# Optimization experiments

Hardware: AMD Instinct MI355X
Metric: run time of the kernel (lower is better)

## Reference

```python
import jax, jax.numpy as jnp
import numpy as np

B = 2
NUM_CLS = 20
NUM_DIM = 256
H = W = 448
FH = FW = 28
K_TOP = 25


def _l2norm(x, eps=1e-12):
    # matches torch F.normalize(dim=1): x / max(||x||, eps); zero rows stay zero
    return x / jnp.maximum(jnp.linalg.norm(x, axis=-1, keepdims=True), eps)


def setup_inputs():
    key = jax.random.key(0)
    k1, k2, k3, k4 = jax.random.split(key, 4)
    fmap = jax.random.normal(k1, (B, NUM_DIM, FH, FW), jnp.float32)
    cam = jax.random.uniform(k2, (B, NUM_CLS, H, W), jnp.float32)
    cls_label = jax.random.randint(k3, (B, NUM_CLS), 0, 2).astype(jnp.float32)
    proj_weight = jax.random.normal(k4, (NUM_CLS, NUM_DIM), jnp.float32) * 0.02
    feature_contrast = jnp.zeros((NUM_CLS, NUM_DIM), jnp.float32)
    return {"fmap": fmap, "cam": cam, "cls_label": cls_label,
            "proj_weight": proj_weight, "feature_contrast": feature_contrast,
            "hig_thre": 0.7, "low_thre": 0.25, "bg_thre": 0.5}


def _forward(fmap, cam, cls_label, proj_weight, feature_contrast, hig_thre, low_thre, bg_thre):
    b, c, h, w = cam.shape
    d = fmap.shape[1]
    dt = fmap.dtype

    # ---- pseudo-label generation (vectorized over b,h,w) ----
    valid_cam = cls_label[:, :, None, None] * cam                       # [B,C,H,W]
    top2_v, top2_i = jax.lax.top_k(jnp.moveaxis(valid_cam, 1, -1), 2)   # [B,H,W,2]
    top1, second = top2_v[..., 0], top2_v[..., 1]
    pseudo = top2_i[..., 0] + 1
    pseudo = jnp.where(top1 < hig_thre, 255, pseudo)
    pseudo = jnp.where(top1 < low_thre, 0, pseudo)
    pseudo = jnp.where(top1 < bg_thre, 0, pseudo)
    pseudo = jnp.where((top1 - second < 0.3) & (top1 > hig_thre), 255, pseudo)

    # ---- upsample features (bilinear, align_corners=False) ----
    fmap_up = jax.image.resize(fmap, (b, d, h, w), 'bilinear')
    fmap_flat = fmap_up.reshape(b, d, h * w)                            # [B,D,HW]
    pseudo_flat = pseudo.reshape(b, h * w)                              # [B,HW]

    # ---- per-class features, both branches computed densely then selected ----
    cls_ids = jnp.arange(c) + 1
    mask = (pseudo_flat[:, None, :] == cls_ids[None, :, None]).astype(dt)  # [B,C,HW]
    counts = mask.sum(-1)                                                  # [B,C]
    feat_mask = jnp.einsum('bcp,bdp->bcd', mask, fmap_flat) / jnp.maximum(counts, 1.0)[:, :, None]
    _, top_idx = jax.lax.top_k(valid_cam.reshape(b, c, h * w), K_TOP)      # [B,C,25]
    gathered = jnp.take_along_axis(fmap_flat[:, None, :, :], top_idx[:, :, None, :], axis=-1)  # [B,C,D,25]
    feat_topk = gathered.mean(-1)                                          # [B,C,D]
    present = cls_label > 0.5                                              # [B,C] bool
    fsm = jnp.where((counts == 0.0)[:, :, None], feat_topk, feat_mask) * present[:, :, None]

    eye_f = jnp.eye(c, dtype=dt)
    eye_b = jnp.eye(c, dtype=bool)

    # ---- sequential per-sample loop (EMA memory bank carried across batch) ----
    def step(carry, xs):
        fc, loss_cls, loss_ccf = carry
        fsm_i, present_i = xs                                    # [C,D], [C]
        fsm_n = _l2norm(fsm_i)
        fc_n = _l2norm(jax.lax.stop_gradient(fc))
        cos = jnp.clip(jnp.abs(fsm_n @ fc_n.T), 1e-5, 1.0 - 1e-5)  # [C,C]
        ident = jnp.diag(present_i.astype(dt))
        loss_ccf = loss_ccf - (ident * jnp.log(cos) + (1.0 - ident) * jnp.log1p(-cos)).mean()
        off_max = jnp.where(eye_b, -jnp.inf, cos).max(axis=1)      # max over j != c
        qualify = present_i & (off_max < 0.6)                      # [C] bool
        p = jax.nn.softmax(fsm_i @ proj_weight.T, axis=-1)         # [C,C]
        logp = jnp.maximum(jnp.log(p), -100.0)
        log1mp = jnp.maximum(jnp.log1p(-p), -100.0)
        term = -(eye_f * logp + (1.0 - eye_f) * log1mp).mean(axis=-1)  # BCE(softmax, onehot) per class
        loss_cls = loss_cls + jnp.sum(jnp.where(qualify, term, 0.0))
        n = qualify.sum().astype(dt)
        loss_cls = jnp.where(n > 0, loss_cls / jnp.maximum(n, 1.0), loss_cls)
        fc = jnp.where(qualify[:, None], 0.95 * fc + 0.05 * jax.lax.stop_gradient(fsm_i), fc)
        return (fc, loss_cls, loss_ccf), None

    zero = jnp.asarray(0.0, dt)
    (_, loss_cls, loss_ccf), _ = jax.lax.scan(step, (feature_contrast, zero, zero), (fsm, present))
    return loss_ccf + loss_cls


def reference(fmap, cam, cls_label, proj_weight, feature_contrast, hig_thre, low_thre, bg_thre):
    return _forward(fmap, cam, cls_label, proj_weight, feature_contrast, hig_thre, low_thre, bg_thre)
```

## Files before the change

### kernel.cpp

```cpp
#include <hip/hip_runtime.h>
#include <cstdint>

#define HW 200704
#define IMG_W 448
#define NCLS 20
#define NDIM 256
#define NB2 784
#define LK 260

#define ASYNC_COPY16(gp, lp)                                                   \
  __builtin_amdgcn_global_load_lds(                                            \
      (const __attribute__((address_space(1))) void*)(gp),                     \
      (__attribute__((address_space(3))) void*)(lp), 16, 0, 0)

__global__ __launch_bounds__(256) void k_front(const float* __restrict__ fmap,
                                               float* __restrict__ fmapT,
                                               const float* __restrict__ cam,
                                               const float* __restrict__ cls_label,
                                               const float* __restrict__ hig_p,
                                               const float* __restrict__ low_p,
                                               const float* __restrict__ bg_p,
                                               float* __restrict__ W) {
  __shared__ float sT[NCLS][256];
  __shared__ int presList[NCLS];
  __shared__ int sNP;
  int tid = threadIdx.x;

  if (blockIdx.x >= 2 * NB2) {
    float (*tile)[33] = (float (*)[33]) & sT[0][0];
    int blk = blockIdx.x - 2 * NB2;
    int b = blk / 200;
    int t = blk % 200;
    int dT = t / 25, sT2 = t % 25;
    int ty = tid >> 5, tx = tid & 31;
#pragma unroll
    for (int r = 0; r < 4; ++r) {
      int d = dT * 32 + ty + r * 8;
      int s = sT2 * 32 + tx;
      if (s < 784) tile[ty + r * 8][tx] = fmap[((size_t)(b * 256 + d)) * 784 + s];
    }
    __syncthreads();
#pragma unroll
    for (int r = 0; r < 4; ++r) {
      int s = sT2 * 32 + ty + r * 8;
      int d = dT * 32 + tx;
      if (s < 784) fmapT[((size_t)(b * 784 + s)) * 256 + d] = tile[tx][ty + r * 8];
    }
    return;
  }

  int b = blockIdx.x / NB2;
  int blkInB = blockIdx.x % NB2;
  int pix0 = blkInB * 256;
  int wave = tid >> 6, lane = tid & 63;

  if (tid < 64) {
    bool pres = (tid < NCLS) && (cls_label[b * NCLS + tid] != 0.0f);
    unsigned long long pm = __ballot(pres);
    if (pres) presList[(int)__popcll(pm & ((1ull << tid) - 1ull))] = tid;
    if (tid == 0) sNP = (int)__popcll(pm);
  }
  __syncthreads();
  int np = sNP;
  const float* camb = cam + (size_t)b * NCLS * HW + pix0;

  for (int k = wave; k < np; k += 4)
    ASYNC_COPY16(camb + (size_t)presList[k] * HW + lane * 4, &sT[k][0]);
  __syncthreads();

  float top1 = -1.0f, sec = -1.0f;
  int cls1 = 0;
  for (int k = 0; k < np; ++k) {
    float x = sT[k][tid];
    bool gt = x > top1;
    sec = gt ? top1 : fmaxf(sec, fminf(x, top1));
    cls1 = gt ? presList[k] : cls1;
    top1 = gt ? x : top1;
  }
  if (np < NCLS) sec = fmaxf(sec, 0.0f);
  float hig = hig_p[0], low = low_p[0], bg = bg_p[0];
  int pix = pix0 + tid;
  int ps = cls1 + 1;
  if (top1 < hig) ps = 255;
  if (top1 < low) ps = 0;
  if (top1 < bg)  ps = 0;
  if ((top1 - sec < 0.3f) && (top1 > hig)) ps = 255;
  if (ps >= 1 && ps <= NCLS) {
    int cls = ps - 1;
    int y = pix / IMG_W, x = pix % IMG_W;
    float sy = (y + 0.5f) * 0.0625f - 0.5f; sy = fminf(fmaxf(sy, 0.0f), 27.0f);
    float sx = (x + 0.5f) * 0.0625f - 0.5f; sx = fminf(fmaxf(sx, 0.0f), 27.0f);
    int fy0 = (int)sy, fx0 = (int)sx;
    int fy1 = min(fy0 + 1, 27), fx1 = min(fx0 + 1, 27);
    float wy = sy - (float)fy0, wx = sx - (float)fx0;
    float* Wb = W + (size_t)(b * NCLS + cls) * 784;
    atomicAdd(&Wb[fy0 * 28 + fx0], (1.0f - wy) * (1.0f - wx));
    atomicAdd(&Wb[fy0 * 28 + fx1], (1.0f - wy) * wx);
    atomicAdd(&Wb[fy1 * 28 + fx0], wy * (1.0f - wx));
    atomicAdd(&Wb[fy1 * 28 + fx1], wy * wx);
  }
}

__global__ __launch_bounds__(1024) void k_feat(const float* __restrict__ fmapT,
                                               const float* __restrict__ cam,
                                               const float* __restrict__ Wg,
                                               const float* __restrict__ cls_label,
                                               float* __restrict__ fsm_g) {
  __shared__ float sW[784];
  __shared__ float sPart[4][256];
  __shared__ float wv[16]; __shared__ int wi[16];
  __shared__ float selV; __shared__ int selI;
  __shared__ int sTop[25];
  __shared__ float sRed[16];
  __shared__ float sCntf;
  int bc = blockIdx.x;
  int b = bc / NCLS;
  int tid = threadIdx.x;
  int dim = tid & 255, part = tid >> 8;
  bool present = (cls_label[bc] != 0.0f);
  const float* fT = fmapT + (size_t)b * 784 * 256;
  float res = 0.0f;

  if (present) {
    for (int s = tid; s < 784; s += 1024) sW[s] = Wg[(size_t)bc * 784 + s];
    __syncthreads();
    {
      float cs = (tid < 784) ? sW[tid] : 0.0f;
      for (int off = 32; off > 0; off >>= 1) cs += __shfl_xor(cs, off, 64);
      if ((tid & 63) == 0) sRed[tid >> 6] = cs;
      __syncthreads();
      if (tid == 0) {
        float s = 0.0f;
        for (int w = 0; w < 16; ++w) s += sRed[w];
        sCntf = s;
      }
      __syncthreads();
    }
    float cntf = sCntf;
    if (cntf > 0.0f) {
      float a0 = 0.0f, a1 = 0.0f, a2 = 0.0f, a3 = 0.0f;
      int s0 = part * 196;
      for (int s = s0; s < s0 + 196; s += 4) {
        a0 += sW[s]     * fT[(size_t)(s)     * 256 + dim];
        a1 += sW[s + 1] * fT[(size_t)(s + 1) * 256 + dim];
        a2 += sW[s + 2] * fT[(size_t)(s + 2) * 256 + dim];
        a3 += sW[s + 3] * fT[(size_t)(s + 3) * 256 + dim];
      }
      sPart[part][dim] = (a0 + a1) + (a2 + a3);
      __syncthreads();
      if (tid < 256)
        res = ((sPart[0][tid] + sPart[1][tid]) + (sPart[2][tid] + sPart[3][tid]))
              / fmaxf(cntf, 1.0f);
    } else {
      const float* camc = cam + (size_t)bc * HW;
      float lastV = 3.0e38f; int lastI = -1;
      for (int r = 0; r < 25; ++r) {
        float bv = -1.0e30f; int bi = 0x7fffffff;
        for (int p = tid; p < HW; p += 1024) {
          float vv2 = camc[p];
          if (((vv2 < lastV) || (vv2 == lastV && p > lastI)) &&
              ((vv2 > bv) || (vv2 == bv && p < bi))) { bv = vv2; bi = p; }
        }
        for (int off = 32; off > 0; off >>= 1) {
          float ov = __shfl_xor(bv, off, 64);
          int   oi = __shfl_xor(bi, off, 64);
          if (ov > bv || (ov == bv && oi < bi)) { bv = ov; bi = oi; }
        }
        if ((tid & 63) == 0) { wv[tid >> 6] = bv; wi[tid >> 6] = bi; }
        __syncthreads();
        if (tid == 0) {
          for (int w = 1; w < 16; ++w)
            if (wv[w] > bv || (wv[w] == bv && wi[w] < bi)) { bv = wv[w]; bi = wi[w]; }
          selV = bv; selI = bi; sTop[r] = bi;
        }
        __syncthreads();
        lastV = selV; lastI = selI;
      }
      float at = 0.0f;
      for (int r = part; r < 25; r += 4) {
        int p = sTop[r];
        int y = p / IMG_W, x = p % IMG_W;
        float sy = (y + 0.5f) * 0.0625f - 0.5f; sy = fminf(fmaxf(sy, 0.0f), 27.0f);
        float sx = (x + 0.5f) * 0.0625f - 0.5f; sx = fminf(fmaxf(sx, 0.0f), 27.0f);
        int fy0 = (int)sy, fx0 = (int)sx;
        int fy1 = min(fy0 + 1, 27), fx1 = min(fx0 + 1, 27);
        float wy = sy - (float)fy0, wx = sx - (float)fx0;
        at += (1.0f - wy) * (1.0f - wx) * fT[(size_t)(fy0 * 28 + fx0) * 256 + dim]
            + (1.0f - wy) * wx          * fT[(size_t)(fy0 * 28 + fx1) * 256 + dim]
            + wy          * (1.0f - wx) * fT[(size_t)(fy1 * 28 + fx0) * 256 + dim]
            + wy          * wx          * fT[(size_t)(fy1 * 28 + fx1) * 256 + dim];
      }
      sPart[part][dim] = at;
      __syncthreads();
      if (tid < 256)
        res = ((sPart[0][tid] + sPart[1][tid]) + (sPart[2][tid] + sPart[3][tid])) * (1.0f / 25.0f);
    }
  }
  if (tid < 256) fsm_g[(size_t)bc * 256 + tid] = res;
}

__global__ __launch_bounds__(1024) void k_loss(const float* __restrict__ fsm_g,
                                               const float* __restrict__ cls_label,
                                               const float* __restrict__ proj_w,
                                               const float* __restrict__ fc_init,
                                               float* __restrict__ out) {
  __shared__ float sFsm[2][NCLS * LK];
  __shared__ float sFc[NCLS * LK], sPw[NCLS * LK];
  __shared__ float sLogit[2][400], sCos[400];
  __shared__ float sBCE[2][NCLS], sRow[NCLS];
  __shared__ float sNormI[2][NCLS], sNormC[NCLS];
  __shared__ int   sZI[2][NCLS], sZC[NCLS], sQual[NCLS];
  __shared__ float sPres[2][NCLS];
  __shared__ float sScal[2];
  int tid = threadIdx.x;

  for (int idx = tid; idx < 2 * NCLS * NDIM; idx += 1024) {
    int b = idx / (NCLS * NDIM);
    int rem = idx - b * NCLS * NDIM;
    sFsm[b][(rem >> 8) * LK + (rem & 255)] = fsm_g[idx];
  }
  for (int idx = tid; idx < NCLS * NDIM; idx += 1024) {
    int r = idx >> 8, d = idx & 255;
    sFc[r * LK + d] = fc_init[idx];
    sPw[r * LK + d] = proj_w[idx];
  }
  if (tid < 40) sPres[tid / NCLS][tid % NCLS] = cls_label[tid];
  if (tid == 0) { sScal[0] = 0.0f; sScal[1] = 0.0f; }
  __syncthreads();

  if (tid < 800) {
    int b = tid / 400, pi = tid % 400;
    int i = pi / NCLS, j = pi % NCLS;
    const float* ra = &sFsm[b][i * LK];
    const float* rb = &sPw[j * LK];
    float a0 = 0, a1 = 0, a2 = 0, a3 = 0, a4 = 0, a5 = 0, a6 = 0, a7 = 0;
    for (int d = 0; d < 256; d += 16) {
      float4 x0 = *(const float4*)&ra[d],      y0 = *(const float4*)&rb[d];
      float4 x1 = *(const float4*)&ra[d + 4],  y1 = *(const float4*)&rb[d + 4];
      float4 x2 = *(const float4*)&ra[d + 8],  y2 = *(const float4*)&rb[d + 8];
      float4 x3 = *(const float4*)&ra[d + 12], y3 = *(const float4*)&rb[d + 12];
      a0 += x0.x * y0.x + x0.y * y0.y;  a1 += x0.z * y0.z + x0.w * y0.w;
      a2 += x1.x * y1.x + x1.y * y1.y;  a3 += x1.z * y1.z + x1.w * y1.w;
      a4 += x2.x * y2.x + x2.y * y2.y;  a5 += x2.z * y2.z + x2.w * y2.w;
      a6 += x3.x * y3.x + x3.y * y3.y;  a7 += x3.z * y3.z + x3.w * y3.w;
    }
    sLogit[b][pi] = ((a0 + a1) + (a2 + a3)) + ((a4 + a5) + (a6 + a7));
  }
  __syncthreads();

  {
    int g = tid >> 3, sub = tid & 7;
    if (g < 60) {
      const float* row = (g < 40) ? &sFsm[g / NCLS][(g % NCLS) * LK] : &sFc[(g - 40) * LK];
      float a0 = 0.0f, a1 = 0.0f, a2 = 0.0f, a3 = 0.0f;
      int d0 = sub * 32;
#pragma unroll
      for (int d = d0; d < d0 + 32; d += 8) {
        float4 x = *(const float4*)&row[d];
        float4 y = *(const float4*)&row[d + 4];
        a0 += x.x * x.x + x.y * x.y;
        a1 += x.z * x.z + x.w * x.w;
        a2 += y.x * y.x + y.y * y.y;
        a3 += y.z * y.z + y.w * y.w;
      }
      float s = (a0 + a1) + (a2 + a3);
      s += __shfl_xor(s, 1, 64);
      s += __shfl_xor(s, 2, 64);
      s += __shfl_xor(s, 4, 64);
      if (sub == 0) {
        if (g < 40) { sNormI[g / NCLS][g % NCLS] = fmaxf(sqrtf(s), 1e-12f); sZI[g / NCLS][g % NCLS] = (s == 0.0f); }
        else { sNormC[g - 40] = fmaxf(sqrtf(s), 1e-12f); sZC[g - 40] = (s == 0.0f); }
      }
    }
  }
  __syncthreads();

  {
    int team = tid >> 5, jj = tid & 31;
    for (int r = team; r < 40; r += 32) {
      int b = r / NCLS, i = r % NCLS;
      float l = (jj < NCLS) ? sLogit[b][i * NCLS + jj] : -3.0e38f;
      float m = l;
#pragma unroll
      for (int off = 1; off < 32; off <<= 1) m = fmaxf(m, __shfl_xor(m, off, 64));
      float e = (jj < NCLS) ? expf(l - m) : 0.0f;
      float S = e;
#pragma unroll
      for (int off = 1; off < 32; off <<= 1) S += __shfl_xor(S, off, 64);
      float term = 0.0f;
      if (jj < NCLS) {
        float p = e / S;
        term = (jj == i) ? fmaxf(logf(p), -100.0f) : fmaxf(log1pf(-p), -100.0f);
      }
#pragma unroll
      for (int off = 1; off < 32; off <<= 1) term += __shfl_xor(term, off, 64);
      if (jj == 0) sBCE[b][i] = -term / 20.0f;
    }
  }
  __syncthreads();

  for (int b = 0; b < 2; ++b) {
    if (b == 1) {
      int g = tid >> 3, sub = tid & 7;
      if (g < NCLS) {
        const float* row = &sFc[g * LK];
        float a0 = 0.0f, a1 = 0.0f, a2 = 0.0f, a3 = 0.0f;
        int d0 = sub * 32;
#pragma unroll
        for (int d = d0; d < d0 + 32; d += 8) {
          float4 x = *(const float4*)&row[d];
          float4 y = *(const float4*)&row[d + 4];
          a0 += x.x * x.x + x.y * x.y;
          a1 += x.z * x.z + x.w * x.w;
          a2 += y.x * y.x + y.y * y.y;
          a3 += y.z * y.z + y.w * y.w;
        }
        float s = (a0 + a1) + (a2 + a3);
        s += __shfl_xor(s, 1, 64);
        s += __shfl_xor(s, 2, 64);
        s += __shfl_xor(s, 4, 64);
        if (sub == 0) { sNormC[g] = fmaxf(sqrtf(s), 1e-12f); sZC[g] = (s == 0.0f); }
      }
      __syncthreads();
    }
    {
      int pair = tid >> 1, sub = tid & 1;
      if (pair < 400) {
        int i = pair / NCLS, j = pair % NCLS;
        float c0;
        if (sZI[b][i] || sZC[j]) c0 = 0.0f;
        else {
          const float* ra = &sFsm[b][i * LK];
          const float* rb = &sFc[j * LK];
          float a0 = 0.0f, a1 = 0.0f, a2 = 0.0f, a3 = 0.0f;
          int d0 = sub * 128;
          for (int d = d0; d < d0 + 128; d += 8) {
            float4 x  = *(const float4*)&ra[d];
            float4 y  = *(const float4*)&rb[d];
            float4 x2 = *(const float4*)&ra[d + 4];
            float4 y2 = *(const float4*)&rb[d + 4];
            a0 += x.x * y.x + x.y * y.y;
            a1 += x.z * y.z + x.w * y.w;
            a2 += x2.x * y2.x + x2.y * y2.y;
            a3 += x2.z * y2.z + x2.w * y2.w;
          }
          float acc = (a0 + a1) + (a2 + a3);
          acc += __shfl_xor(acc, 1, 64);
          c0 = fabsf(acc / (sNormI[b][i] * sNormC[j]));
        }
        if (sub == 0) sCos[pair] = fminf(fmaxf(c0, 1e-5f), 1.0f - 1e-5f);
      }
    }
    __syncthreads();
    {
      int i = tid >> 5, jj = tid & 31;
      if (i < NCLS) {
        float pres = (sPres[b][i] > 0.5f) ? 1.0f : 0.0f;
        float contrib = 0.0f, omv = -3.0e38f;
        if (jj < NCLS) {
          float c0 = sCos[i * NCLS + jj];
          float ident = (jj == i) ? pres : 0.0f;
          contrib = ident * logf(c0) + (1.0f - ident) * log1pf(-c0);
          if (jj != i) omv = c0;
        }
#pragma unroll
        for (int off = 1; off < 32; off <<= 1) {
          contrib += __shfl_xor(contrib, off, 64);
          omv = fmaxf(omv, __shfl_xor(omv, off, 64));
        }
        if (jj == 0) { sRow[i] = contrib; sQual[i] = (pres > 0.5f && omv < 0.6f) ? 1 : 0; }
      }
    }
    __syncthreads();
    if (tid == 0) {
      float s = 0.0f;
      for (int r = 0; r < NCLS; ++r) s += sRow[r];
      sScal[0] -= s / 400.0f;
      float add = 0.0f; int nq = 0;
      for (int r = 0; r < NCLS; ++r) if (sQual[r]) { add += sBCE[b][r]; nq++; }
      float lc = sScal[1] + add;
      if (nq > 0) lc = lc / fmaxf((float)nq, 1.0f);
      sScal[1] = lc;
    }
    for (int idx = tid; idx < NCLS * NDIM; idx += 1024) {
      int r = idx >> 8, d = idx & 255;
      if (sQual[r]) sFc[r * LK + d] = 0.95f * sFc[r * LK + d] + 0.05f * sFsm[b][r * LK + d];
    }
    __syncthreads();
  }
  if (tid == 0) out[0] = sScal[0] + sScal[1];
}

extern "C" void kernel_launch(void* const* d_in, const int* in_sizes, int n_in,
                              void* d_out, int out_size, void* d_ws, size_t ws_size,
                              hipStream_t stream) {
  const float* fmap      = (const float*)d_in[0];
  const float* cam       = (const float*)d_in[1];
  const float* cls_label = (const float*)d_in[2];
  const float* proj_w    = (const float*)d_in[3];
  const float* fc_init   = (const float*)d_in[4];
  const float* hig       = (const float*)d_in[5];
  const float* low       = (const float*)d_in[6];
  const float* bg        = (const float*)d_in[7];
  float* out = (float*)d_out;

  char* ws = (char*)d_ws;
  float* W       = (float*)(ws);
  float* fsm     = (float*)(ws + 125440);
  float* fmapT   = (float*)(ws + 166400);

  hipMemsetAsync(ws, 0, 125440, stream);
  k_front<<<2 * NB2 + 400,  256, 0, stream>>>(fmap, fmapT, cam, cls_label,
                                              hig, low, bg, W);
  k_feat <<<           40, 1024, 0, stream>>>(fmapT, cam, W, cls_label, fsm);
  k_loss <<<            1, 1024, 0, stream>>>(fsm, cls_label, proj_w, fc_init, out);
}
```

Measured before the change: 128.1 us.

## Split feature pooling across more blocks and use per-wave cam loads

```diff
diff --git a/kernel.cpp b/kernel.cpp
--- a/kernel.cpp
+++ b/kernel.cpp
@@ -8,10 +8,10 @@
 #define NB2 784
 #define LK 260
 
-#define ASYNC_COPY16(gp, lp)                                                   \
+#define ASYNC_COPY4(gp, lp)                                                    \
   __builtin_amdgcn_global_load_lds(                                            \
       (const __attribute__((address_space(1))) void*)(gp),                     \
-      (__attribute__((address_space(3))) void*)(lp), 16, 0, 0)
+      (__attribute__((address_space(3))) void*)(lp), 4, 0, 0)
 
 __global__ __launch_bounds__(256) void k_front(const float* __restrict__ fmap,
                                                float* __restrict__ fmapT,
@@ -22,8 +22,6 @@
                                                const float* __restrict__ bg_p,
                                                float* __restrict__ W) {
   __shared__ float sT[NCLS][256];
-  __shared__ int presList[NCLS];
-  __shared__ int sNP;
   int tid = threadIdx.x;
 
   if (blockIdx.x >= 2 * NB2) {
@@ -54,28 +52,33 @@
   int pix0 = blkInB * 256;
   int wave = tid >> 6, lane = tid & 63;
 
-  if (tid < 64) {
-    bool pres = (tid < NCLS) && (cls_label[b * NCLS + tid] != 0.0f);
-    unsigned long long pm = __ballot(pres);
-    if (pres) presList[(int)__popcll(pm & ((1ull << tid) - 1ull))] = tid;
-    if (tid == 0) sNP = (int)__popcll(pm);
-  }
-  __syncthreads();
-  int np = sNP;
-  const float* camb = cam + (size_t)b * NCLS * HW + pix0;
-
-  for (int k = wave; k < np; k += 4)
-    ASYNC_COPY16(camb + (size_t)presList[k] * HW + lane * 4, &sT[k][0]);
-  __syncthreads();
+  bool pres = (lane < NCLS) && (cls_label[b * NCLS + lane] != 0.0f);
+  unsigned long long pm = __ballot(pres);
+  unsigned mask = (unsigned)(pm & 0xFFFFFu);
+  int np = __popc(mask);
+  const float* camb = cam + (size_t)b * NCLS * HW + pix0 + wave * 64 + lane;
+
+  {
+    unsigned m = mask;
+    for (int k = 0; k < np; ++k) {
+      int c = __builtin_ctz(m); m &= m - 1u;
+      ASYNC_COPY4(camb + (size_t)c * HW, &sT[k][wave * 64]);
+    }
+  }
+  __builtin_amdgcn_s_waitcnt(0);
 
   float top1 = -1.0f, sec = -1.0f;
   int cls1 = 0;
-  for (int k = 0; k < np; ++k) {
-    float x = sT[k][tid];
-    bool gt = x > top1;
-    sec = gt ? top1 : fmaxf(sec, fminf(x, top1));
-    cls1 = gt ? presList[k] : cls1;
-    top1 = gt ? x : top1;
+  {
+    unsigned m = mask;
+    for (int k = 0; k < np; ++k) {
+      int c = __builtin_ctz(m); m &= m - 1u;
+      float x = sT[k][tid];
+      bool gt = x > top1;
+      sec = gt ? top1 : fmaxf(sec, fminf(x, top1));
+      cls1 = gt ? c : cls1;
+      top1 = gt ? x : top1;
+    }
   }
   if (np < NCLS) sec = fmaxf(sec, 0.0f);
   float hig = hig_p[0], low = low_p[0], bg = bg_p[0];
@@ -101,83 +104,95 @@
   }
 }
 
-__global__ __launch_bounds__(1024) void k_feat(const float* __restrict__ fmapT,
-                                               const float* __restrict__ cam,
-                                               const float* __restrict__ Wg,
-                                               const float* __restrict__ cls_label,
-                                               float* __restrict__ fsm_g) {
+__global__ __launch_bounds__(512) void k_feat(const float* __restrict__ fmapT,
+                                              const float* __restrict__ cam,
+                                              const float* __restrict__ Wg,
+                                              const float* __restrict__ cls_label,
+                                              float* __restrict__ P,
+                                              float* __restrict__ S,
+                                              float* __restrict__ cntW) {
   __shared__ float sW[784];
-  __shared__ float sPart[4][256];
-  __shared__ float wv[16]; __shared__ int wi[16];
+  __shared__ float sH[2][256];
+  __shared__ float sRed[8];
+  __shared__ float sCntf;
+  __shared__ float wv[8]; __shared__ int wi[8];
   __shared__ float selV; __shared__ int selI;
   __shared__ int sTop[25];
-  __shared__ float sRed[16];
-  __shared__ float sCntf;
-  int bc = blockIdx.x;
+  int bc = blockIdx.x >> 2, part = blockIdx.x & 3;
   int b = bc / NCLS;
   int tid = threadIdx.x;
-  int dim = tid & 255, part = tid >> 8;
-  bool present = (cls_label[bc] != 0.0f);
+  int dim = tid & 255, h = tid >> 8;
+  if (cls_label[bc] == 0.0f) return;
+
+  for (int s = tid; s < 784; s += 512) sW[s] = Wg[(size_t)bc * 784 + s];
+  __syncthreads();
+  {
+    float cs = sW[tid >= 512 ? 0 : tid];
+    cs = (tid < 512) ? sW[tid] : 0.0f;
+    if (tid < 272) cs += sW[tid + 512];
+    for (int off = 32; off > 0; off >>= 1) cs += __shfl_xor(cs, off, 64);
+    if ((tid & 63) == 0) sRed[tid >> 6] = cs;
+    __syncthreads();
+    if (tid == 0) {
+      float s = 0.0f;
+      for (int w = 0; w < 8; ++w) s += sRed[w];
+      sCntf = s;
+    }
+    __syncthreads();
+  }
+  float cntf = sCntf;
   const float* fT = fmapT + (size_t)b * 784 * 256;
-  float res = 0.0f;
-
-  if (present) {
-    for (int s = tid; s < 784; s += 1024) sW[s] = Wg[(size_t)bc * 784 + s];
-    __syncthreads();
-    {
-      float cs = (tid < 784) ? sW[tid] : 0.0f;
-      for (int off = 32; off > 0; off >>= 1) cs += __shfl_xor(cs, off, 64);
-      if ((tid & 63) == 0) sRed[tid >> 6] = cs;
-      __syncthreads();
-      if (tid == 0) {
-        float s = 0.0f;
-        for (int w = 0; w < 16; ++w) s += sRed[w];
-        sCntf = s;
-      }
-      __syncthreads();
-    }
-    float cntf = sCntf;
-    if (cntf > 0.0f) {
-      float a0 = 0.0f, a1 = 0.0f, a2 = 0.0f, a3 = 0.0f;
-      int s0 = part * 196;
+
+  if (cntf > 0.0f) {
+    int s0 = part * 196;
+    if (h == 0) {
+      float a0 = 0.0f, a1 = 0.0f;
       for (int s = s0; s < s0 + 196; s += 4) {
         a0 += sW[s]     * fT[(size_t)(s)     * 256 + dim];
         a1 += sW[s + 1] * fT[(size_t)(s + 1) * 256 + dim];
+      }
+      sH[0][dim] = a0 + a1;
+    } else {
+      float a2 = 0.0f, a3 = 0.0f;
+      for (int s = s0; s < s0 + 196; s += 4) {
         a2 += sW[s + 2] * fT[(size_t)(s + 2) * 256 + dim];
         a3 += sW[s + 3] * fT[(size_t)(s + 3) * 256 + dim];
       }
-      sPart[part][dim] = (a0 + a1) + (a2 + a3);
+      sH[1][dim] = a2 + a3;
+    }
+    __syncthreads();
+    if (tid < 256)
+      P[(size_t)(bc * 4 + part) * 256 + tid] = sH[0][tid] + sH[1][tid];
+    if (part == 0 && tid == 0) cntW[bc] = cntf;
+  } else if (part == 0) {
+    if (tid == 0) cntW[bc] = 0.0f;
+    const float* camc = cam + (size_t)bc * HW;
+    float lastV = 3.0e38f; int lastI = -1;
+    for (int r = 0; r < 25; ++r) {
+      float bv = -1.0e30f; int bi = 0x7fffffff;
+      for (int p = tid; p < HW; p += 512) {
+        float vv2 = camc[p];
+        if (((vv2 < lastV) || (vv2 == lastV && p > lastI)) &&
+            ((vv2 > bv) || (vv2 == bv && p < bi))) { bv = vv2; bi = p; }
+      }
+      for (int off = 32; off > 0; off >>= 1) {
+        float ov = __shfl_xor(bv, off, 64);
+        int   oi = __shfl_xor(bi, off, 64);
+        if (ov > bv || (ov == bv && oi < bi)) { bv = ov; bi = oi; }
+      }
+      if ((tid & 63) == 0) { wv[tid >> 6] = bv; wi[tid >> 6] = bi; }
       __syncthreads();
-      if (tid < 256)
-        res = ((sPart[0][tid] + sPart[1][tid]) + (sPart[2][tid] + sPart[3][tid]))
-              / fmaxf(cntf, 1.0f);
-    } else {
-      const float* camc = cam + (size_t)bc * HW;
-      float lastV = 3.0e38f; int lastI = -1;
+      if (tid == 0) {
+        for (int w = 1; w < 8; ++w)
+          if (wv[w] > bv || (wv[w] == bv && wi[w] < bi)) { bv = wv[w]; bi = wi[w]; }
+        selV = bv; selI = bi; sTop[r] = bi;
+      }
+      __syncthreads();
+      lastV = selV; lastI = selI;
+    }
+    if (tid < 256) {
+      float at = 0.0f;
       for (int r = 0; r < 25; ++r) {
-        float bv = -1.0e30f; int bi = 0x7fffffff;
-        for (int p = tid; p < HW; p += 1024) {
-          float vv2 = camc[p];
-          if (((vv2 < lastV) || (vv2 == lastV && p > lastI)) &&
-              ((vv2 > bv) || (vv2 == bv && p < bi))) { bv = vv2; bi = p; }
-        }
-        for (int off = 32; off > 0; off >>= 1) {
-          float ov = __shfl_xor(bv, off, 64);
-          int   oi = __shfl_xor(bi, off, 64);
-          if (ov > bv || (ov == bv && oi < bi)) { bv = ov; bi = oi; }
-        }
-        if ((tid & 63) == 0) { wv[tid >> 6] = bv; wi[tid >> 6] = bi; }
-        __syncthreads();
-        if (tid == 0) {
-          for (int w = 1; w < 16; ++w)
-            if (wv[w] > bv || (wv[w] == bv && wi[w] < bi)) { bv = wv[w]; bi = wi[w]; }
-          selV = bv; selI = bi; sTop[r] = bi;
-        }
-        __syncthreads();
-        lastV = selV; lastI = selI;
-      }
-      float at = 0.0f;
-      for (int r = part; r < 25; r += 4) {
         int p = sTop[r];
         int y = p / IMG_W, x = p % IMG_W;
         float sy = (y + 0.5f) * 0.0625f - 0.5f; sy = fminf(fmaxf(sy, 0.0f), 27.0f);
@@ -185,21 +200,19 @@
         int fy0 = (int)sy, fx0 = (int)sx;
         int fy1 = min(fy0 + 1, 27), fx1 = min(fx0 + 1, 27);
         float wy = sy - (float)fy0, wx = sx - (float)fx0;
-        at += (1.0f - wy) * (1.0f - wx) * fT[(size_t)(fy0 * 28 + fx0) * 256 + dim]
-            + (1.0f - wy) * wx          * fT[(size_t)(fy0 * 28 + fx1) * 256 + dim]
-            + wy          * (1.0f - wx) * fT[(size_t)(fy1 * 28 + fx0) * 256 + dim]
-            + wy          * wx          * fT[(size_t)(fy1 * 28 + fx1) * 256 + dim];
-      }
-      sPart[part][dim] = at;
-      __syncthreads();
-      if (tid < 256)
-        res = ((sPart[0][tid] + sPart[1][tid]) + (sPart[2][tid] + sPart[3][tid])) * (1.0f / 25.0f);
-    }
-  }
-  if (tid < 256) fsm_g[(size_t)bc * 256 + tid] = res;
+        at += (1.0f - wy) * (1.0f - wx) * fT[(size_t)(fy0 * 28 + fx0) * 256 + tid]
+            + (1.0f - wy) * wx          * fT[(size_t)(fy0 * 28 + fx1) * 256 + tid]
+            + wy          * (1.0f - wx) * fT[(size_t)(fy1 * 28 + fx0) * 256 + tid]
+            + wy          * wx          * fT[(size_t)(fy1 * 28 + fx1) * 256 + tid];
+      }
+      S[(size_t)bc * 256 + tid] = at * (1.0f / 25.0f);
+    }
+  }
 }
 
-__global__ __launch_bounds__(1024) void k_loss(const float* __restrict__ fsm_g,
+__global__ __launch_bounds__(1024) void k_loss(const float* __restrict__ P,
+                                               const float* __restrict__ S,
+                                               const float* __restrict__ cntW,
                                                const float* __restrict__ cls_label,
                                                const float* __restrict__ proj_w,
                                                const float* __restrict__ fc_init,
@@ -215,9 +228,18 @@
   int tid = threadIdx.x;
 
   for (int idx = tid; idx < 2 * NCLS * NDIM; idx += 1024) {
-    int b = idx / (NCLS * NDIM);
-    int rem = idx - b * NCLS * NDIM;
-    sFsm[b][(rem >> 8) * LK + (rem & 255)] = fsm_g[idx];
+    int bc = idx >> 8, d = idx & 255;
+    float v = 0.0f;
+    if (cls_label[bc] != 0.0f) {
+      float c = cntW[bc];
+      if (c > 0.0f) {
+        const float* p = P + (size_t)bc * 1024 + d;
+        v = ((p[0] + p[256]) + (p[512] + p[768])) / fmaxf(c, 1.0f);
+      } else {
+        v = S[(size_t)bc * 256 + d];
+      }
+    }
+    sFsm[bc / NCLS][(bc % NCLS) * LK + d] = v;
   }
   for (int idx = tid; idx < NCLS * NDIM; idx += 1024) {
     int r = idx >> 8, d = idx & 255;
@@ -284,12 +306,12 @@
 #pragma unroll
       for (int off = 1; off < 32; off <<= 1) m = fmaxf(m, __shfl_xor(m, off, 64));
       float e = (jj < NCLS) ? expf(l - m) : 0.0f;
-      float S = e;
-#pragma unroll
-      for (int off = 1; off < 32; off <<= 1) S += __shfl_xor(S, off, 64);
+      float sS = e;
+#pragma unroll
+      for (int off = 1; off < 32; off <<= 1) sS += __shfl_xor(sS, off, 64);
       float term = 0.0f;
       if (jj < NCLS) {
-        float p = e / S;
+        float p = e / sS;
         term = (jj == i) ? fmaxf(logf(p), -100.0f) : fmaxf(log1pf(-p), -100.0f);
       }
 #pragma unroll
@@ -405,13 +427,15 @@
   float* out = (float*)d_out;
 
   char* ws = (char*)d_ws;
-  float* W       = (float*)(ws);
-  float* fsm     = (float*)(ws + 125440);
-  float* fmapT   = (float*)(ws + 166400);
+  float* W     = (float*)(ws);
+  float* cntW  = (float*)(ws + 125440);
+  float* P     = (float*)(ws + 125600);
+  float* S     = (float*)(ws + 289440);
+  float* fmapT = (float*)(ws + 330400);
 
   hipMemsetAsync(ws, 0, 125440, stream);
   k_front<<<2 * NB2 + 400,  256, 0, stream>>>(fmap, fmapT, cam, cls_label,
                                               hig, low, bg, W);
-  k_feat <<<           40, 1024, 0, stream>>>(fmapT, cam, W, cls_label, fsm);
-  k_loss <<<            1, 1024, 0, stream>>>(fsm, cls_label, proj_w, fc_init, out);
+  k_feat <<<          160,  512, 0, stream>>>(fmapT, cam, W, cls_label, P, S, cntW);
+  k_loss <<<            1, 1024, 0, stream>>>(P, S, cntW, cls_label, proj_w, fc_init, out);
 }
```

New measurement: 123.7 us. 1.04x faster.
